# Kernel optimization log

Measured on AMD Instinct MI355X. Metric: run time of the kernel, lower is better.

Reference implementation:

```python
import jax, jax.numpy as jnp
import numpy as np

N = 65536      # nodes (256x256 grid)
E = 1048576    # edges (avg degree 16)
T_IN = 10      # TIME_STEPS_IN
L = 64         # LATENT_DIMS
MID = 128      # LATENT_DIMS * MLP_RATIO
GD = 2         # grid dims


def _lin_init(key, fan_in, fan_out):
    kw, kb = jax.random.split(key)
    s = 1.0 / np.sqrt(fan_in)
    W = jax.random.uniform(kw, (fan_in, fan_out), jnp.float32, -s, s)
    b = jax.random.uniform(kb, (fan_out,), jnp.float32, -s, s)
    return W, b


def setup_inputs() -> dict:
    key = jax.random.key(0)
    ks = jax.random.split(key, 10)
    x = jax.random.normal(ks[0], (N, T_IN), jnp.float32)
    grid = jax.random.uniform(ks[1], (N, GD), jnp.float32)
    edge_index = jax.random.randint(ks[2], (2, E), 0, N, jnp.int64)
    W_proj1, b_proj1 = _lin_init(ks[3], T_IN + GD, MID)
    W_proj2, b_proj2 = _lin_init(ks[4], MID, L)
    Wk, bk = _lin_init(ks[5], 2 * L + 2 * GD + 1, L)   # K edge MLP (single linear)
    Ww, bw = _lin_init(ks[6], L, L)                     # W node MLP (single linear)
    W_dec1, b_dec1 = _lin_init(ks[7], L, MID)
    W_dec2, b_dec2 = _lin_init(ks[8], MID, 1)
    return {"x": x, "grid": grid, "edge_index": edge_index,
            "W_proj1": W_proj1, "b_proj1": b_proj1, "W_proj2": W_proj2, "b_proj2": b_proj2,
            "Wk": Wk, "bk": bk, "Ww": Ww, "bw": bw,
            "W_dec1": W_dec1, "b_dec1": b_dec1, "W_dec2": W_dec2, "b_dec2": b_dec2}


def _gelu(x):
    return jax.nn.gelu(x, approximate=False)  # torch F.gelu default = exact erf


def reference(x, grid, edge_index, W_proj1, b_proj1, W_proj2, b_proj2,
              Wk, bk, Ww, bw, W_dec1, b_dec1, W_dec2, b_dec2):
    # project: cat(x, grid) -> Linear -> GELU -> Linear
    h = jnp.concatenate([x, grid], axis=-1)               # [N, T_IN+2]
    h = _gelu(h @ W_proj1 + b_proj1) @ W_proj2 + b_proj2  # [N, L]

    # message passing block (PyG source_to_target: j = row 0, i = row 1)
    src = edge_index[0]
    dst = edge_index[1]
    x_j = h[src]                                          # [E, L]
    x_i = h[dst]                                          # [E, L]
    g_j = grid[src]                                       # [E, 2]
    g_i = grid[dst]                                       # [E, 2]
    dist = jnp.sqrt(jnp.sum(jnp.square(g_i - g_j), axis=-1, keepdims=True))  # [E, 1]
    ef = jnp.concatenate([dist, g_i, g_j, x_i, x_j], axis=-1)  # [E, 2L+5]
    msg = ef @ Wk + bk                                    # [E, L]
    aggr = jax.ops.segment_sum(msg, dst, num_segments=N)  # [N, L]
    h = _gelu(h @ Ww + bw + aggr)                         # update

    # decode: Linear -> GELU -> Linear
    out = _gelu(h @ W_dec1 + b_dec1) @ W_dec2 + b_dec2    # [N, 1]
    return out
```

## Files before the change

### kernel.cpp

```cpp
#include <hip/hip_runtime.h>
#include <hip/hip_fp16.h>

static __device__ __forceinline__ float gelu(float x) {
    return 0.5f * x * (1.0f + erff(x * 0.70710678118654752f));
}

#define CAPR 32

typedef _Float16 v8h __attribute__((ext_vector_type(8)));
typedef float    v4f __attribute__((ext_vector_type(4)));
typedef int      v4i __attribute__((ext_vector_type(4)));
union F8 { uint4 u; v8h v; _Float16 f[8]; };

static __device__ __forceinline__ void acc8(float* a, uint4 u) {
    float2 f0 = __half22float2(*(__half2*)&u.x);
    float2 f1 = __half22float2(*(__half2*)&u.y);
    float2 f2 = __half22float2(*(__half2*)&u.z);
    float2 f3 = __half22float2(*(__half2*)&u.w);
    a[0] += f0.x; a[1] += f0.y; a[2] += f1.x; a[3] += f1.y;
    a[4] += f2.x; a[5] += f2.y; a[6] += f3.x; a[7] += f3.y;
}

static __device__ __forceinline__ uint4 pack8(const float* v) {
    __half2 p0 = __floats2half2_rn(v[0], v[1]);
    __half2 p1 = __floats2half2_rn(v[2], v[3]);
    __half2 p2 = __floats2half2_rn(v[4], v[5]);
    __half2 p3 = __floats2half2_rn(v[6], v[7]);
    uint4 u;
    u.x = *(unsigned*)&p0; u.y = *(unsigned*)&p1;
    u.z = *(unsigned*)&p2; u.w = *(unsigned*)&p3;
    return u;
}

__global__ void __launch_bounds__(256, 8)
k_scat(const int* __restrict__ ei, int* __restrict__ cnt,
       unsigned short* __restrict__ ssrc, int N, int E, int scatB)
{
    int tid = threadIdx.x;
    int p = blockIdx.x & 7;
    int c = blockIdx.x >> 3;
    const v4i* s4 = (const v4i*)ei;
    const v4i* d4 = (const v4i*)(ei + E);
    int g4 = (E / (scatB >> 3)) >> 2;
    int base4 = c * g4;
    int shift = 31 - __clz(N >> 3);
#pragma unroll 8
    for (int g = 0; g < g4 / 256; g++) {
        int idx = base4 + g * 256 + tid;
        v4i d = __builtin_nontemporal_load(&d4[idx]);
        v4i s = __builtin_nontemporal_load(&s4[idx]);
        int q;
        if ((d[0] >> shift) == p) {
            q = atomicAdd(&cnt[(d[0] << 1) + 0], 1);
            if (q < CAPR) ssrc[((size_t)d[0] << 6) + q] = (unsigned short)s[0];
        }
        if ((d[1] >> shift) == p) {
            q = atomicAdd(&cnt[(d[1] << 1) + 1], 1);
            if (q < CAPR) ssrc[((size_t)d[1] << 6) + 32 + q] = (unsigned short)s[1];
        }
        if ((d[2] >> shift) == p) {
            q = atomicAdd(&cnt[(d[2] << 1) + 0], 1);
            if (q < CAPR) ssrc[((size_t)d[2] << 6) + q] = (unsigned short)s[2];
        }
        if ((d[3] >> shift) == p) {
            q = atomicAdd(&cnt[(d[3] << 1) + 1], 1);
            if (q < CAPR) ssrc[((size_t)d[3] << 6) + 32 + q] = (unsigned short)s[3];
        }
    }
}

__global__ void __launch_bounds__(256, 4)
k_enc(const float* __restrict__ x,
      const float* __restrict__ grid,
      const float* __restrict__ W1,
      const float* __restrict__ b1,
      const float* __restrict__ W2,
      const float* __restrict__ b2,
      __half* __restrict__ h16, int N)
{
    __shared__ uint4 tabW2[1024];
    __shared__ __half wmids[4 * 16 * 136];
    int tid = threadIdx.x;
    int eb = blockIdx.x;
    int lane = tid & 63, wave = tid >> 6;
    int m = lane & 15, quad = lane >> 4;

    F8 w1f[8];
#pragma unroll
    for (int nt = 0; nt < 8; nt++) {
        int col = nt * 16 + m;
        int k0 = quad << 3;
#pragma unroll
        for (int j = 0; j < 8; j++)
            w1f[nt].f[j] = (k0 + j < 12) ? (_Float16)W1[(k0 + j) * 128 + col] : (_Float16)0.f;
    }

    for (int idx = tid; idx < 1024; idx += 256) {
        int l2 = idx & 63, nt = (idx >> 6) & 3, kc = idx >> 8;
        int col = nt * 16 + (l2 & 15);
        int k0 = kc * 32 + ((l2 >> 4) << 3);
        F8 f;
#pragma unroll
        for (int j = 0; j < 8; j++) f.f[j] = (_Float16)W2[(k0 + j) * 64 + col];
        tabW2[idx] = f.u;
    }
    __syncthreads();

    __half* wm = &wmids[wave * 16 * 136];

    for (int t = 0; t < 2; t++) {
        int tile = eb * 8 + wave * 2 + t;
        int base = tile * 16;
        int n = base + m;
        F8 a1;
#pragma unroll
        for (int j = 0; j < 8; j++) a1.f[j] = (_Float16)0.f;
        if (quad == 0) {
            float2 x0 = *(const float2*)&x[(size_t)n * 10 + 0];
            float2 x1 = *(const float2*)&x[(size_t)n * 10 + 2];
            float2 x2 = *(const float2*)&x[(size_t)n * 10 + 4];
            float2 x3 = *(const float2*)&x[(size_t)n * 10 + 6];
            a1.f[0] = (_Float16)x0.x; a1.f[1] = (_Float16)x0.y;
            a1.f[2] = (_Float16)x1.x; a1.f[3] = (_Float16)x1.y;
            a1.f[4] = (_Float16)x2.x; a1.f[5] = (_Float16)x2.y;
            a1.f[6] = (_Float16)x3.x; a1.f[7] = (_Float16)x3.y;
        } else if (quad == 1) {
            float2 x4 = *(const float2*)&x[(size_t)n * 10 + 8];
            float2 g  = *(const float2*)&grid[(size_t)n * 2];
            a1.f[0] = (_Float16)x4.x; a1.f[1] = (_Float16)x4.y;
            a1.f[2] = (_Float16)g.x;  a1.f[3] = (_Float16)g.y;
        }
#pragma unroll
        for (int nt = 0; nt < 8; nt++) {
            int col = nt * 16 + m;
            float b = b1[col];
            v4f acc = {b, b, b, b};
            acc = __builtin_amdgcn_mfma_f32_16x16x32_f16(a1.v, w1f[nt].v, acc, 0, 0, 0);
#pragma unroll
            for (int reg = 0; reg < 4; reg++)
                wm[(quad * 4 + reg) * 136 + col] = __float2half(gelu(acc[reg]));
        }
        __syncthreads();

        F8 a2[4];
#pragma unroll
        for (int kc = 0; kc < 4; kc++)
            a2[kc].u = *(const uint4*)&wm[m * 136 + kc * 32 + quad * 8];
#pragma unroll
        for (int nt = 0; nt < 4; nt++) {
            int col = nt * 16 + m;
            float b = b2[col];
            v4f acc = {b, b, b, b};
#pragma unroll
            for (int kc = 0; kc < 4; kc++) {
                F8 bf; bf.u = tabW2[kc * 256 + nt * 64 + lane];
                acc = __builtin_amdgcn_mfma_f32_16x16x32_f16(a2[kc].v, bf.v, acc, 0, 0, 0);
            }
#pragma unroll
            for (int reg = 0; reg < 4; reg++)
                h16[(size_t)(base + quad * 4 + reg) * 64 + col] = __float2half(acc[reg]);
        }
        __syncthreads();
    }
}

__global__ void k_gather(const __half* __restrict__ h16,
                         const float* __restrict__ grid,
                         const unsigned short* __restrict__ ssrc,
                         const int* __restrict__ cnt,
                         __half* __restrict__ sum_h16, float* __restrict__ sum_g,
                         float* __restrict__ sum_d, int N)
{
    int tid = blockIdx.x * blockDim.x + threadIdx.x;
    int n = tid >> 3;
    int l = tid & 7;
    if (n >= N) return;
    int2 cv = *(const int2*)&cnt[n << 1];
    const uint4* h8 = (const uint4*)h16;
    float a[8] = {0,0,0,0,0,0,0,0};
    float sgx = 0.f, sgy = 0.f, sd = 0.f;
    float gix = grid[2 * n], giy = grid[2 * n + 1];
#pragma unroll
    for (int r = 0; r < 2; r++) {
        int dg = min((r == 0) ? cv.x : cv.y, CAPR);
        const unsigned short* sr = ssrc + ((size_t)n << 6) + (r << 5);
        for (int i = 0; i < dg; i += 4) {
            ushort4 sv = *(const ushort4*)&sr[i];
            int sx = sv.x, sy = sv.y, sz = sv.z, sw = sv.w;
            int rem = dg - i;
            if (rem < 4) {
                if (rem <= 1) sy = sx;
                if (rem <= 2) sz = sx;
                sw = (rem <= 3) ? sx : sw;
            }
            uint4 u0 = h8[(size_t)sx * 8 + l];
            uint4 u1 = h8[(size_t)sy * 8 + l];
            uint4 u2 = h8[(size_t)sz * 8 + l];
            uint4 u3 = h8[(size_t)sw * 8 + l];
            acc8(a, u0);
            if (rem > 1) acc8(a, u1);
            if (rem > 2) acc8(a, u2);
            if (rem > 3) acc8(a, u3);
            if (l < 4 && i + l < dg) {
                int sj = (l == 0) ? sx : (l == 1) ? sy : (l == 2) ? sz : sw;
                float2 g = *(const float2*)&grid[2 * sj];
                float dx = gix - g.x, dy = giy - g.y;
                sd += sqrtf(dx * dx + dy * dy);
                sgx += g.x; sgy += g.y;
            }
        }
    }
    sd  += __shfl_xor(sd, 1);  sd  += __shfl_xor(sd, 2);  sd  += __shfl_xor(sd, 4);
    sgx += __shfl_xor(sgx, 1); sgx += __shfl_xor(sgx, 2); sgx += __shfl_xor(sgx, 4);
    sgy += __shfl_xor(sgy, 1); sgy += __shfl_xor(sgy, 2); sgy += __shfl_xor(sgy, 4);
    ((uint4*)(sum_h16 + (size_t)n * 64))[l] = pack8(a);
    if (l == 0) { sum_d[n] = sd; sum_g[2 * n] = sgx; sum_g[2 * n + 1] = sgy; }
}

__global__ void __launch_bounds__(256, 1)
k_updec(const __half* __restrict__ h16, const __half* __restrict__ sum_h16,
        const float* __restrict__ sum_g, const float* __restrict__ sum_d,
        const int* __restrict__ cnt, const float* __restrict__ grid,
        const float* __restrict__ Wk, const float* __restrict__ bk,
        const float* __restrict__ Ww, const float* __restrict__ bw,
        const float* __restrict__ Wd1, const float* __restrict__ bd1,
        const float* __restrict__ Wd2, const float* __restrict__ bd2,
        float* __restrict__ out, int N)
{
    __shared__ uint4 tabW[512];
    __shared__ uint4 tabC[512];
    __shared__ uint4 tabD[512];
    __shared__ uint4 tabV[256];
    __shared__ uint4 tabE[1024];
    __shared__ __half h2t[4 * 16 * 72];
    int tid = threadIdx.x;

    for (int idx = tid; idx < 512; idx += 256) {
        int lane = idx & 63, nt = (idx >> 6) & 3, kc = idx >> 8;
        int col = nt * 16 + (lane & 15);
        int kr  = kc * 32 + ((lane >> 4) << 3);
        F8 fw, fc, fd;
#pragma unroll
        for (int j = 0; j < 8; j++) {
            fw.f[j] = (_Float16)Ww[(kr + j) * 64 + col];
            fc.f[j] = (_Float16)Wk[(size_t)(5 + kr + j) * 64 + col];
            fd.f[j] = (_Float16)Wk[(size_t)(69 + kr + j) * 64 + col];
        }
        tabW[idx] = fw.u; tabC[idx] = fc.u; tabD[idx] = fd.u;
    }
    if (tid < 256) {
        int lane = tid & 63, nt = tid >> 6;
        int col = nt * 16 + (lane & 15);
        F8 fv;
#pragma unroll
        for (int j = 0; j < 8; j++) fv.f[j] = (_Float16)0.f;
        if ((lane >> 4) == 0) {
            fv.f[0] = (_Float16)bw[col];
            fv.f[1] = (_Float16)bk[col];
            fv.f[2] = (_Float16)Wk[col];
            fv.f[3] = (_Float16)Wk[64 + col];
            fv.f[4] = (_Float16)Wk[128 + col];
            fv.f[5] = (_Float16)Wk[192 + col];
            fv.f[6] = (_Float16)Wk[256 + col];
        }
        tabV[tid] = fv.u;
    }
    for (int idx = tid; idx < 1024; idx += 256) {
        int lane = idx & 63, nt = (idx >> 6) & 7, kc = idx >> 9;
        int col = nt * 16 + (lane & 15);
        int kr  = kc * 32 + ((lane >> 4) << 3);
        F8 f;
#pragma unroll
        for (int j = 0; j < 8; j++) f.f[j] = (_Float16)Wd1[(kr + j) * 128 + col];
        tabE[idx] = f.u;
    }
    __syncthreads();

    int lane = tid & 63, wave = tid >> 6;
    int m = lane & 15, quad = lane >> 4;
    const uint4* h8 = (const uint4*)h16;
    const uint4* s8 = (const uint4*)sum_h16;
    __half* wt = &h2t[wave * 16 * 72];
    float bd2v = bd2[0];

    for (int t = 0; t < 2; t++) {
        int tile = blockIdx.x * 8 + wave * 2 + t;
        int base = tile * 16;
        int n = base + m;
        int2 cv = *(const int2*)&cnt[n << 1];
        float deg = (float)(min(cv.x, CAPR) + min(cv.y, CAPR));
        float sd  = sum_d[n];
        float sgx = sum_g[2 * n], sgy = sum_g[2 * n + 1];
        float gix = grid[2 * n] * deg, giy = grid[2 * n + 1] * deg;

        F8 ah0, ah1, as0, as1, ahd0, ahd1, au;
        ah0.u = h8[(size_t)n * 8 + quad];
        ah1.u = h8[(size_t)n * 8 + 4 + quad];
        as0.u = s8[(size_t)n * 8 + quad];
        as1.u = s8[(size_t)n * 8 + 4 + quad];
        _Float16 dh = (_Float16)deg;
#pragma unroll
        for (int j = 0; j < 8; j++) { ahd0.f[j] = ah0.f[j] * dh; ahd1.f[j] = ah1.f[j] * dh; }
        float z = (quad == 0) ? 1.f : 0.f;
        au.f[0] = (_Float16)z;          au.f[1] = (_Float16)(deg * z);
        au.f[2] = (_Float16)(sd * z);   au.f[3] = (_Float16)(gix * z);
        au.f[4] = (_Float16)(giy * z);  au.f[5] = (_Float16)(sgx * z);
        au.f[6] = (_Float16)(sgy * z);  au.f[7] = (_Float16)0.f;

#pragma unroll
        for (int nt = 0; nt < 4; nt++) {
            F8 bv, bw0, bw1, bc0, bc1, bd0, bd1f;
            bv.u  = tabV[nt * 64 + lane];
            bw0.u = tabW[nt * 64 + lane];       bw1.u = tabW[256 + nt * 64 + lane];
            bc0.u = tabC[nt * 64 + lane];       bc1.u = tabC[256 + nt * 64 + lane];
            bd0.u = tabD[nt * 64 + lane];       bd1f.u = tabD[256 + nt * 64 + lane];
            v4f acc = {0.f, 0.f, 0.f, 0.f};
            acc = __builtin_amdgcn_mfma_f32_16x16x32_f16(au.v,   bv.v,   acc, 0, 0, 0);
            acc = __builtin_amdgcn_mfma_f32_16x16x32_f16(ah0.v,  bw0.v,  acc, 0, 0, 0);
            acc = __builtin_amdgcn_mfma_f32_16x16x32_f16(ah1.v,  bw1.v,  acc, 0, 0, 0);
            acc = __builtin_amdgcn_mfma_f32_16x16x32_f16(ahd0.v, bc0.v,  acc, 0, 0, 0);
            acc = __builtin_amdgcn_mfma_f32_16x16x32_f16(ahd1.v, bc1.v,  acc, 0, 0, 0);
            acc = __builtin_amdgcn_mfma_f32_16x16x32_f16(as0.v,  bd0.v,  acc, 0, 0, 0);
            acc = __builtin_amdgcn_mfma_f32_16x16x32_f16(as1.v,  bd1f.v, acc, 0, 0, 0);
#pragma unroll
            for (int reg = 0; reg < 4; reg++)
                wt[(quad * 4 + reg) * 72 + m + 16 * nt] = __float2half(gelu(acc[reg]));
        }
        __syncthreads();

        F8 dh0, dh1;
        dh0.u = *(const uint4*)&wt[m * 72 + quad * 8];
        dh1.u = *(const uint4*)&wt[m * 72 + 32 + quad * 8];
        float p[4] = {0.f, 0.f, 0.f, 0.f};
#pragma unroll
        for (int nt = 0; nt < 8; nt++) {
            int col = m + 16 * nt;
            float b = bd1[col];
            float w2 = Wd2[col];
            F8 b0, b1;
            b0.u = tabE[nt * 64 + lane];
            b1.u = tabE[512 + nt * 64 + lane];
            v4f acc = {b, b, b, b};
            acc = __builtin_amdgcn_mfma_f32_16x16x32_f16(dh0.v, b0.v, acc, 0, 0, 0);
            acc = __builtin_amdgcn_mfma_f32_16x16x32_f16(dh1.v, b1.v, acc, 0, 0, 0);
#pragma unroll
            for (int reg = 0; reg < 4; reg++) p[reg] += gelu(acc[reg]) * w2;
        }
#pragma unroll
        for (int reg = 0; reg < 4; reg++) {
            p[reg] += __shfl_xor(p[reg], 1);
            p[reg] += __shfl_xor(p[reg], 2);
            p[reg] += __shfl_xor(p[reg], 4);
            p[reg] += __shfl_xor(p[reg], 8);
        }
        if (m == 0) {
#pragma unroll
            for (int reg = 0; reg < 4; reg++)
                out[base + quad * 4 + reg] = p[reg] + bd2v;
        }
        __syncthreads();
    }
}

extern "C" void kernel_launch(void* const* d_in, const int* in_sizes, int n_in,
                              void* d_out, int out_size, void* d_ws, size_t ws_size,
                              hipStream_t stream)
{
    const float* x    = (const float*)d_in[0];
    const float* grid = (const float*)d_in[1];
    const int*   ei   = (const int*)d_in[2];
    const float* W1   = (const float*)d_in[3];
    const float* b1   = (const float*)d_in[4];
    const float* W2   = (const float*)d_in[5];
    const float* b2   = (const float*)d_in[6];
    const float* Wk   = (const float*)d_in[7];
    const float* bk   = (const float*)d_in[8];
    const float* Ww   = (const float*)d_in[9];
    const float* bw   = (const float*)d_in[10];
    const float* Wd1  = (const float*)d_in[11];
    const float* bd1  = (const float*)d_in[12];
    const float* Wd2  = (const float*)d_in[13];
    const float* bd2  = (const float*)d_in[14];
    float* out = (float*)d_out;

    int N = in_sizes[0] / 10;
    int E = in_sizes[2] / 2;

    char* ws = (char*)d_ws;
    size_t o_h16  = 0;
    size_t o_sh16 = o_h16  + (size_t)N * 64 * 2;
    size_t o_sumg = o_sh16 + (size_t)N * 64 * 2;
    size_t o_sumd = o_sumg + (size_t)N * 2 * 4;
    size_t o_cnt  = o_sumd + (size_t)N * 4;
    size_t o_ssrc = o_cnt  + (size_t)N * 2 * 4;

    __half* h16     = (__half*)(ws + o_h16);
    __half* sum_h16 = (__half*)(ws + o_sh16);
    float* sum_g = (float*)(ws + o_sumg);
    float* sum_d = (float*)(ws + o_sumd);
    int*   cnt   = (int*)  (ws + o_cnt);
    unsigned short* ssrc = (unsigned short*)(ws + o_ssrc);

    hipMemsetAsync(cnt, 0, (size_t)N * 2 * 4, stream);

    int scatB = E / (256 * 4);
    int encB  = (N / 16) / 8;
    k_scat<<<dim3(scatB), dim3(256), 0, stream>>>(ei, cnt, ssrc, N, E, scatB);
    k_enc<<<dim3(encB), dim3(256), 0, stream>>>(x, grid, W1, b1, W2, b2, h16, N);
    k_gather<<<dim3((N * 8 + 255) / 256), dim3(256), 0, stream>>>(h16, grid, ssrc, cnt,
                                                                   sum_h16, sum_g, sum_d, N);
    int tiles = N / 16;
    k_updec<<<dim3(tiles / 8), dim3(256), 0, stream>>>(h16, sum_h16, sum_g, sum_d, cnt,
                                                       grid, Wk, bk, Ww, bw,
                                                       Wd1, bd1, Wd2, bd2, out, N);
}
```

Baseline: 209.0 us.

## Pre-bin edges by destination partition and fuse binning with encoder launch

Adds a preprocessing pass that reads each edge once, bins it by destination partition in shared memory, and appends packed (dst,src) words to per-partition global queues. The scatter kernel then reads only its own partition's queue instead of every block rescanning the full edge list eight times. The binning blocks are merged into the encoder launch so the two run concurrently. The cost is an extra write and read of the packed edge stream through a workspace buffer aliased onto sum_h16. It also risks dropping edges if a block's bin exceeds 272 entries or a queue exceeds its capacity.

```diff
diff --git a/kernel.cpp b/kernel.cpp
--- a/kernel.cpp
+++ b/kernel.cpp
@@ -6,6 +6,7 @@
 }
 
 #define CAPR 32
+#define QCAP (160 * 1024)
 
 typedef _Float16 v8h __attribute__((ext_vector_type(8)));
 typedef float    v4f __attribute__((ext_vector_type(4)));
@@ -32,56 +33,49 @@
     return u;
 }
 
-__global__ void __launch_bounds__(256, 8)
-k_scat(const int* __restrict__ ei, int* __restrict__ cnt,
-       unsigned short* __restrict__ ssrc, int N, int E, int scatB)
+__global__ void __launch_bounds__(256, 4)
+k_prep_enc(const int* __restrict__ ei, int* __restrict__ qcnt, int* __restrict__ qdata,
+           const float* __restrict__ x, const float* __restrict__ grid,
+           const float* __restrict__ W1, const float* __restrict__ b1,
+           const float* __restrict__ W2, const float* __restrict__ b2,
+           __half* __restrict__ h16, int N, int E, int prepB)
 {
+    __shared__ __align__(16) unsigned char smraw[33792];
     int tid = threadIdx.x;
-    int p = blockIdx.x & 7;
-    int c = blockIdx.x >> 3;
-    const v4i* s4 = (const v4i*)ei;
-    const v4i* d4 = (const v4i*)(ei + E);
-    int g4 = (E / (scatB >> 3)) >> 2;
-    int base4 = c * g4;
-    int shift = 31 - __clz(N >> 3);
-#pragma unroll 8
-    for (int g = 0; g < g4 / 256; g++) {
-        int idx = base4 + g * 256 + tid;
-        v4i d = __builtin_nontemporal_load(&d4[idx]);
-        v4i s = __builtin_nontemporal_load(&s4[idx]);
-        int q;
-        if ((d[0] >> shift) == p) {
-            q = atomicAdd(&cnt[(d[0] << 1) + 0], 1);
-            if (q < CAPR) ssrc[((size_t)d[0] << 6) + q] = (unsigned short)s[0];
-        }
-        if ((d[1] >> shift) == p) {
-            q = atomicAdd(&cnt[(d[1] << 1) + 1], 1);
-            if (q < CAPR) ssrc[((size_t)d[1] << 6) + 32 + q] = (unsigned short)s[1];
-        }
-        if ((d[2] >> shift) == p) {
-            q = atomicAdd(&cnt[(d[2] << 1) + 0], 1);
-            if (q < CAPR) ssrc[((size_t)d[2] << 6) + q] = (unsigned short)s[2];
-        }
-        if ((d[3] >> shift) == p) {
-            q = atomicAdd(&cnt[(d[3] << 1) + 1], 1);
-            if (q < CAPR) ssrc[((size_t)d[3] << 6) + 32 + q] = (unsigned short)s[3];
-        }
-    }
-}
-
-__global__ void __launch_bounds__(256, 4)
-k_enc(const float* __restrict__ x,
-      const float* __restrict__ grid,
-      const float* __restrict__ W1,
-      const float* __restrict__ b1,
-      const float* __restrict__ W2,
-      const float* __restrict__ b2,
-      __half* __restrict__ h16, int N)
-{
-    __shared__ uint4 tabW2[1024];
-    __shared__ __half wmids[4 * 16 * 136];
-    int tid = threadIdx.x;
-    int eb = blockIdx.x;
+
+    if ((int)blockIdx.x < prepB) {
+        int (*bins)[272] = (int(*)[272])smraw;
+        int* bcnt  = (int*)(smraw + 8704);
+        int* bbase = (int*)(smraw + 8736);
+        if (tid < 8) bcnt[tid] = 0;
+        __syncthreads();
+        int e4 = blockIdx.x * 256 + tid;
+        const v4i* s4 = (const v4i*)ei;
+        const v4i* d4 = (const v4i*)(ei + E);
+        v4i d = __builtin_nontemporal_load(&d4[e4]);
+        v4i s = __builtin_nontemporal_load(&s4[e4]);
+        int shift = 31 - __clz(N >> 3);
+#pragma unroll
+        for (int j = 0; j < 4; j++) {
+            int p = d[j] >> shift;
+            int pos = atomicAdd(&bcnt[p], 1);
+            if (pos < 272) bins[p][pos] = (d[j] << 16) | (s[j] & 0xFFFF);
+        }
+        __syncthreads();
+        if (tid < 8) bbase[tid] = atomicAdd(&qcnt[tid], min(bcnt[tid], 272));
+        __syncthreads();
+#pragma unroll
+        for (int p = 0; p < 8; p++) {
+            int c = min(bcnt[p], 272), b = bbase[p];
+            for (int i = tid; i < c; i += 256)
+                qdata[p * QCAP + b + i] = bins[p][i];
+        }
+        return;
+    }
+
+    uint4*  tabW2 = (uint4*)smraw;
+    __half* wmids = (__half*)(smraw + 16384);
+    int eb = blockIdx.x - prepB;
     int lane = tid & 63, wave = tid >> 6;
     int m = lane & 15, quad = lane >> 4;
 
@@ -161,6 +155,31 @@
                 h16[(size_t)(base + quad * 4 + reg) * 64 + col] = __float2half(acc[reg]);
         }
         __syncthreads();
+    }
+}
+
+__global__ void __launch_bounds__(256, 8)
+k_scat(const int* __restrict__ qcnt, const int* __restrict__ qdata,
+       int* __restrict__ cnt, unsigned short* __restrict__ ssrc)
+{
+    int tid = threadIdx.x;
+    int p = blockIdx.x & 7;
+    int c = blockIdx.x >> 3;
+    int qn = min(qcnt[p], QCAP);
+    const int* q = qdata + p * QCAP;
+    for (int base = c * 1024; base < qn; base += 128 * 1024) {
+#pragma unroll
+        for (int k = 0; k < 4; k++) {
+            int idx = base + k * 256 + tid;
+            if (idx < qn) {
+                unsigned v = (unsigned)q[idx];
+                int dst = v >> 16;
+                int src = v & 0xFFFF;
+                int rep = idx & 1;
+                int qq = atomicAdd(&cnt[(dst << 1) + rep], 1);
+                if (qq < CAPR) ssrc[((size_t)dst << 6) + (rep << 5) + qq] = (unsigned short)src;
+            }
+        }
     }
 }
 
@@ -392,21 +411,26 @@
     size_t o_sumg = o_sh16 + (size_t)N * 64 * 2;
     size_t o_sumd = o_sumg + (size_t)N * 2 * 4;
     size_t o_cnt  = o_sumd + (size_t)N * 4;
-    size_t o_ssrc = o_cnt  + (size_t)N * 2 * 4;
+    size_t o_qcnt = o_cnt  + (size_t)N * 2 * 4;
+    size_t o_ssrc = o_qcnt + 1024;
 
     __half* h16     = (__half*)(ws + o_h16);
     __half* sum_h16 = (__half*)(ws + o_sh16);
+    int*   qdata = (int*)  (ws + o_sh16);
     float* sum_g = (float*)(ws + o_sumg);
     float* sum_d = (float*)(ws + o_sumd);
     int*   cnt   = (int*)  (ws + o_cnt);
+    int*   qcnt  = (int*)  (ws + o_qcnt);
     unsigned short* ssrc = (unsigned short*)(ws + o_ssrc);
 
-    hipMemsetAsync(cnt, 0, (size_t)N * 2 * 4, stream);
-
-    int scatB = E / (256 * 4);
+    hipMemsetAsync(cnt, 0, (size_t)N * 2 * 4 + 1024, stream);
+
+    int prepB = E / 1024;
     int encB  = (N / 16) / 8;
-    k_scat<<<dim3(scatB), dim3(256), 0, stream>>>(ei, cnt, ssrc, N, E, scatB);
-    k_enc<<<dim3(encB), dim3(256), 0, stream>>>(x, grid, W1, b1, W2, b2, h16, N);
+    k_prep_enc<<<dim3(prepB + encB), dim3(256), 0, stream>>>(ei, qcnt, qdata,
+                                                             x, grid, W1, b1, W2, b2,
+                                                             h16, N, E, prepB);
+    k_scat<<<dim3(1024), dim3(256), 0, stream>>>(qcnt, qdata, cnt, ssrc);
     k_gather<<<dim3((N * 8 + 255) / 256), dim3(256), 0, stream>>>(h16, grid, ssrc, cnt,
                                                                    sum_h16, sum_g, sum_d, N);
     int tiles = N / 16;
```

Measured after the change: 219.6 us. 5.0% more time.
